# Optimization experiments

Hardware: AMD Instinct MI355X
Metric: run time of the kernel (lower is better)

The kernel has to match this reference:

```python
import jax, jax.numpy as jnp
import numpy as np

E = 304   # embedding size
H = 304   # hidden size
D = 61    # dict_size
B = 256   # batch
T = 512   # frame_num
P = 68    # max_phn_num


def _gru_cell(h, x, Wih, Whh, bih, bhh):
    # PyTorch GRU cell: gates ordered (r, z, n)
    gi = x @ Wih.T + bih            # [B, 3H]
    gh = h @ Whh.T + bhh            # [B, 3H]
    i_r, i_z, i_n = jnp.split(gi, 3, axis=-1)
    h_r, h_z, h_n = jnp.split(gh, 3, axis=-1)
    r = jax.nn.sigmoid(i_r + h_r)
    z = jax.nn.sigmoid(i_z + h_z)
    n = jnp.tanh(i_n + r * h_n)
    return (1.0 - z) * n + z * h


def _run_gru(xs, h0, Wih, Whh, bih, bhh):
    # xs: [B, L, E] -> outputs [B, L, H], final hidden [B, H]
    def step(h, x):
        h = _gru_cell(h, x, Wih, Whh, bih, bhh)
        return h, h
    h_last, outs = jax.lax.scan(step, h0, jnp.swapaxes(xs, 0, 1))
    return jnp.swapaxes(outs, 0, 1), h_last


def setup_inputs() -> dict:
    key = jax.random.key(0)
    ks = jax.random.split(key, 12)
    s = 1.0 / np.sqrt(H)
    u = lambda k, shp: jax.random.uniform(k, shp, jnp.float32, -s, s)
    return {
        'input': jax.random.normal(ks[0], (B, T, E), jnp.float32),
        'target': jax.random.randint(ks[1], (B, P, 1), 0, D),
        'teacher_forcing': 1,
        'enc_Wih': u(ks[2], (3 * H, E)),
        'enc_Whh': u(ks[3], (3 * H, H)),
        'enc_bih': u(ks[4], (3 * H,)),
        'enc_bhh': u(ks[5], (3 * H,)),
        'emb': jax.random.normal(ks[6], (D, E), jnp.float32),
        'dec_Wih': u(ks[7], (3 * H, E)),
        'dec_Whh': u(ks[8], (3 * H, H)),
        'dec_bih': u(ks[9], (3 * H,)),
        'dec_bhh': u(ks[10], (3 * H,)),
        'lin_W': u(ks[11], (D, H)),
        'lin_b': jnp.zeros((D,), jnp.float32),
    }


def reference(input, target, teacher_forcing, enc_Wih, enc_Whh, enc_bih, enc_bhh,
              emb, dec_Wih, dec_Whh, dec_bih, dec_bhh, lin_W, lin_b):
    batch = input.shape[0]
    h0 = jnp.zeros((batch, H), input.dtype)
    # Encoder: the python loop over frames is mathematically a full GRU scan
    enc_outs, enc_h = _run_gru(input, h0, enc_Wih, enc_Whh, enc_bih, enc_bhh)
    # Decoder (teacher_forcing == 1): input tokens are [0, target[:,1], ..., target[:,P-1]]
    toks = jnp.concatenate(
        [jnp.zeros((batch, 1), target.dtype), target[:, 1:, 0]], axis=1)  # [B, P]
    dec_x = emb[toks]                                                      # [B, P, E]
    dec_outs, _ = _run_gru(dec_x, enc_h, dec_Wih, dec_Whh, dec_bih, dec_bhh)
    logits = dec_outs @ lin_W.T + lin_b        # [B, P, D]
    softmaxs = jax.nn.softmax(logits, axis=-1)
    softmax_cal = softmaxs[:, :-1, :].reshape(-1, D)
    target_cal = target[:, 1:, :].reshape(-1)
    asr_outputs = jnp.argmax(softmaxs[:, :-1, :], axis=2)[:, :, None]
    return softmax_cal, target_cal, asr_outputs
```

## Files before the change

### kernel.cpp

```cpp
#include <hip/hip_runtime.h>
#include <math.h>

#define B_   256
#define E_   304
#define H_   304
#define T_   512
#define P_   68
#define PD   67
#define D_   61
#define NCB  16
#define NBG  16
#define RB   16
#define CBH  19
#define GC   57
#define NSTEP (T_ + PD)
#define HW   152
#define BLK_ULL (RB * HW)
#define LROW 328
#define LROWU 164
#define NKS  10
#define SC_LO 2048.0f
#define SC_INV 4.8828125e-4f

typedef unsigned long long ull;
typedef _Float16 half8 __attribute__((ext_vector_type(8)));
typedef _Float16 half2v __attribute__((ext_vector_type(2)));
typedef float f32x4 __attribute__((ext_vector_type(4)));

__global__ __launch_bounds__(256, 1) void gru_persist(
    const float* __restrict__ input,
    const int*   __restrict__ target,
    const float* __restrict__ emb,
    const float* __restrict__ eWih, const float* __restrict__ eWhh,
    const float* __restrict__ ebih, const float* __restrict__ ebhh,
    const float* __restrict__ dWih, const float* __restrict__ dWhh,
    const float* __restrict__ dbih, const float* __restrict__ dbhh,
    float* hbuf,
    float* __restrict__ dec_outs,
    int* ctr)
{
    __shared__ _Float16 opH[2][RB * LROW];
    __shared__ _Float16 opL[2][RB * LROW];
    __shared__ float red0[64 * 17], red1[64 * 17];
    __shared__ float bi_l[2][GC], bh_l[2][GC];

    const int tid  = threadIdx.x;
    const int L    = blockIdx.x;
    const int xcd  = L & 7;
    const int yy   = L >> 3;
    const int cb   = yy & 15;
    const int bg   = ((yy >> 4) << 3) | xcd;
    const int r0   = bg * RB;
    const int c0h  = cb * CBH;
    const int wv   = tid >> 6;
    const int lane = tid & 63;
    int* ctrp = ctr + bg * 32;

    half8 wih_h[NKS], wih_l[NKS], whh_h[NKS], whh_l[NKS];

    auto packw = [&](const float* W, half8* wh, half8* wl) {
        int c = wv * 16 + (lane & 15);
        bool valid = (c < GC);
        int g = valid ? c / CBH : 0, j19 = valid ? c - (c / CBH) * CBH : 0;
        const float* wp = W + (size_t)(g * H_ + c0h + j19) * 304;
        int grp = (lane >> 4) * 8;
        #pragma unroll
        for (int ks = 0; ks < NKS; ++ks) {
            half8 vh, vl;
            #pragma unroll
            for (int j = 0; j < 8; ++j) {
                int k = ks * 32 + grp + j;
                float v = (valid && k < 304) ? wp[k] : 0.f;
                _Float16 hi = (_Float16)v;
                float rres = v - (float)hi;
                vh[j] = hi;
                vl[j] = (_Float16)(rres * SC_LO);
            }
            wh[ks] = vh; wl[ks] = vl;
        }
    };

    auto gemm = [&](const _Float16* aH, const _Float16* aL,
                    const half8* wh, const half8* wl, float* red) {
        const int base = (lane & 15) * LROW + (lane >> 4) * 8;
        f32x4 a0 = {0.f, 0.f, 0.f, 0.f}, a1 = a0, a2 = a0;
        #pragma unroll
        for (int ks = 0; ks < NKS; ++ks) {
            half8 Ah = *(const half8*)&aH[base + ks * 32];
            half8 Al = *(const half8*)&aL[base + ks * 32];
            a0 = __builtin_amdgcn_mfma_f32_16x16x32_f16(Ah, wh[ks], a0, 0, 0, 0);
            a1 = __builtin_amdgcn_mfma_f32_16x16x32_f16(Ah, wl[ks], a1, 0, 0, 0);
            a2 = __builtin_amdgcn_mfma_f32_16x16x32_f16(Al, wh[ks], a2, 0, 0, 0);
        }
        f32x4 r = a0 + (a1 + a2) * SC_INV;
        int rb = (wv * 16 + (lane & 15)) * 17 + (lane >> 4) * 4;
        #pragma unroll
        for (int i = 0; i < 4; ++i) red[rb + i] = r[i];
    };

    auto cvtstore = [&](ull u, int plane, int idx) {
        float a0 = __uint_as_float((unsigned)u);
        float a1 = __uint_as_float((unsigned)(u >> 32));
        _Float16 h0 = (_Float16)a0, h1 = (_Float16)a1;
        float r0f = a0 - (float)h0, r1f = a1 - (float)h1;
        half2v vh; vh.x = h0; vh.y = h1;
        half2v vl; vl.x = (_Float16)(r0f * SC_LO); vl.y = (_Float16)(r1f * SC_LO);
        ((half2v*)&opH[plane][0])[idx] = vh;
        ((half2v*)&opL[plane][0])[idx] = vl;
    };

    packw(eWih, wih_h, wih_l);
    packw(eWhh, whh_h, whh_l);
    if (tid < GC) {
        int g = tid / CBH, j = tid - (tid / CBH) * CBH;
        bi_l[0][tid] = ebih[g * H_ + c0h + j];
        bh_l[0][tid] = ebhh[g * H_ + c0h + j];
        bi_l[1][tid] = dbih[g * H_ + c0h + j];
        bh_l[1][tid] = dbhh[g * H_ + c0h + j];
    }

    for (int f = tid; f < RB * LROW; f += 256) {
        ((unsigned*)opH)[f] = 0u;
        ((unsigned*)opL)[f] = 0u;
    }
    __syncthreads();
    {
        const ull* xin = (const ull*)input;
        #pragma unroll
        for (int i = 0; i < 10; ++i) {
            int f = tid + 256 * i;
            if (i < 9 || f < BLK_ULL) {
                int rr = f / HW, q = f - (f / HW) * HW;
                cvtstore(xin[(size_t)(r0 + rr) * T_ * HW + q], 0, rr * LROWU + q);
            }
        }
    }
    __syncthreads();
    gemm(opH[0], opL[0], wih_h, wih_l, red0);
    ull xr[10];
    {
        const ull* xin = (const ull*)input;
        #pragma unroll
        for (int i = 0; i < 10; ++i) {
            int f = tid + 256 * i;
            if (i < 9 || f < BLK_ULL) {
                int rr = f / HW, q = f - (f / HW) * HW;
                xr[i] = xin[((size_t)(r0 + rr) * T_ + 1) * HW + q];
            }
        }
    }

    for (int s = 0; s < NSTEP; ++s) {
        __syncthreads();
        const bool enc = (s < T_);
        if (s == T_) packw(dWhh, whh_h, whh_l);

        ull hreg[10];
        if (s > 0) {
            const ull* hsrc = (const ull*)(hbuf + (size_t)(s & 1) * (B_ * H_))
                              + (size_t)r0 * HW;
            #pragma unroll
            for (int i = 0; i < 10; ++i) {
                int f = tid + 256 * i;
                if (i < 9 || f < BLK_ULL)
                    hreg[i] = __hip_atomic_load(hsrc + f, __ATOMIC_RELAXED,
                                                __HIP_MEMORY_SCOPE_AGENT);
            }
        }
        if (s + 1 < NSTEP) {
            #pragma unroll
            for (int i = 0; i < 10; ++i) {
                int f = tid + 256 * i;
                if (i < 9 || f < BLK_ULL) {
                    int rr = f / HW, q = f - (f / HW) * HW;
                    cvtstore(xr[i], 0, rr * LROWU + q);
                }
            }
        }
        if (s > 0) {
            #pragma unroll
            for (int i = 0; i < 10; ++i) {
                int f = tid + 256 * i;
                if (i < 9 || f < BLK_ULL) {
                    int rr = f / HW, q = f - (f / HW) * HW;
                    cvtstore(hreg[i], 1, rr * LROWU + q);
                }
            }
        }
        if (s + 2 < NSTEP) {
            if (s + 2 < T_) {
                const ull* xin = (const ull*)input;
                #pragma unroll
                for (int i = 0; i < 10; ++i) {
                    int f = tid + 256 * i;
                    if (i < 9 || f < BLK_ULL) {
                        int rr = f / HW, q = f - (f / HW) * HW;
                        xr[i] = xin[((size_t)(r0 + rr) * T_ + (s + 2)) * HW + q];
                    }
                }
            } else {
                const ull* eb = (const ull*)emb;
                int p2 = s + 2 - T_;
                #pragma unroll
                for (int i = 0; i < 10; ++i) {
                    int f = tid + 256 * i;
                    if (i < 9 || f < BLK_ULL) {
                        int rr = f / HW, q = f - (f / HW) * HW;
                        int tok = (p2 == 0) ? 0 : target[(r0 + rr) * P_ + p2];
                        xr[i] = eb[(size_t)tok * HW + q];
                    }
                }
            }
        }
        __syncthreads();

        gemm(opH[1], opL[1], whh_h, whh_l, red1);
        __syncthreads();

        float* hdst = hbuf + (size_t)((s + 1) & 1) * (B_ * H_);
        for (int o = tid; o < RB * CBH; o += 256) {
            int rr = o / CBH, j = o - (o / CBH) * CBH;
            int col = c0h + j;
            int ph = enc ? 0 : 1;
            float Gi[3], Gh[3];
            #pragma unroll
            for (int g = 0; g < 3; ++g) {
                int c = g * CBH + j;
                Gi[g] = red0[c * 17 + rr] + bi_l[ph][c];
                Gh[g] = red1[c * 17 + rr] + bh_l[ph][c];
            }
            float rg = 1.f / (1.f + expf(-(Gi[0] + Gh[0])));
            float zg = 1.f / (1.f + expf(-(Gi[1] + Gh[1])));
            float ng = tanhf(Gi[2] + rg * Gh[2]);
            float hv = (float)opH[1][rr * LROW + col]
                     + (float)opL[1][rr * LROW + col] * SC_INV;
            float hnew = (1.f - zg) * ng + zg * hv;
            __hip_atomic_store(&hdst[(size_t)(r0 + rr) * H_ + col], hnew,
                               __ATOMIC_RELAXED, __HIP_MEMORY_SCOPE_AGENT);
            if (!enc)
                dec_outs[((size_t)(r0 + rr) * PD + (s - T_)) * H_ + col] = hnew;
        }
        __syncthreads();

        if (s + 1 < NSTEP) {
            if (tid == 0)
                __hip_atomic_fetch_add(ctrp, 1, __ATOMIC_RELAXED,
                                       __HIP_MEMORY_SCOPE_AGENT);
            if (s + 1 == T_) packw(dWih, wih_h, wih_l);
            gemm(opH[0], opL[0], wih_h, wih_l, red0);
            if (tid == 0) {
                int tgt = NCB * (s + 1);
                while (__hip_atomic_load(ctrp, __ATOMIC_RELAXED,
                                         __HIP_MEMORY_SCOPE_AGENT) < tgt)
                    __builtin_amdgcn_s_sleep(1);
            }
        }
    }
}

__global__ __launch_bounds__(256) void logits_softmax(
    const float* __restrict__ dec_outs,
    const float* __restrict__ linW,
    const float* __restrict__ linb,
    const int* __restrict__ target,
    float* __restrict__ out)
{
    __shared__ float wsm[H_][64];
    __shared__ float rs[4][H_];
    const int tid = threadIdx.x;
    const int wv = tid >> 6, l = tid & 63;

    for (int f = tid; f < H_ * 64; f += 256) {
        int k = f >> 6, ll = f & 63;
        wsm[k][ll] = (ll < D_) ? linW[(size_t)ll * H_ + k] : 0.f;
    }
    const int r = blockIdx.x * 4 + wv;
    const float* rowp = dec_outs + (size_t)r * H_;
    for (int k = l; k < H_; k += 64) rs[wv][k] = rowp[k];
    __syncthreads();

    float acc = -1e30f;
    if (l < D_) {
        acc = linb[l];
        #pragma unroll 4
        for (int k = 0; k < H_; ++k) acc += rs[wv][k] * wsm[k][l];
    }
    float m = acc;
    for (int off = 32; off; off >>= 1) m = fmaxf(m, __shfl_xor(m, off));
    float e = (l < D_) ? expf(acc - m) : 0.f;
    float s = e;
    for (int off = 32; off; off >>= 1) s += __shfl_xor(s, off);
    float av = acc; int ai = l;
    for (int off = 32; off; off >>= 1) {
        float ov = __shfl_xor(av, off);
        int oi = __shfl_xor(ai, off);
        if (ov > av || (ov == av && oi < ai)) { av = ov; ai = oi; }
    }
    const int b = r / PD, p = r - (r / PD) * PD;
    const size_t OFF1 = (size_t)B_ * PD * D_;
    const size_t OFF2 = OFF1 + (size_t)B_ * PD;
    if (l < D_)        out[(size_t)r * D_ + l] = e / s;
    else if (l == D_)  out[OFF1 + r] = (float)target[b * P_ + p + 1];
    else if (l == D_ + 1) out[OFF2 + r] = (float)ai;
}

extern "C" void kernel_launch(void* const* d_in, const int* in_sizes, int n_in,
                              void* d_out, int out_size, void* d_ws, size_t ws_size,
                              hipStream_t stream)
{
    const float* input  = (const float*)d_in[0];
    const int*   target = (const int*)d_in[1];
    const float* eWih = (const float*)d_in[3];
    const float* eWhh = (const float*)d_in[4];
    const float* ebih = (const float*)d_in[5];
    const float* ebhh = (const float*)d_in[6];
    const float* emb  = (const float*)d_in[7];
    const float* dWih = (const float*)d_in[8];
    const float* dWhh = (const float*)d_in[9];
    const float* dbih = (const float*)d_in[10];
    const float* dbhh = (const float*)d_in[11];
    const float* linW = (const float*)d_in[12];
    const float* linb = (const float*)d_in[13];
    float* out = (float*)d_out;

    int*   ctr      = (int*)d_ws;
    float* hbuf     = (float*)d_ws + 1024;
    float* dec_outs = hbuf + 2 * (size_t)B_ * H_;

    (void)hipMemsetAsync(ctr, 0, 1024 * sizeof(int), stream);

    gru_persist<<<dim3(256), 256, 0, stream>>>(
        input, target, emb,
        eWih, eWhh, ebih, ebhh,
        dWih, dWhh, dbih, dbhh,
        hbuf, dec_outs, ctr);

    logits_softmax<<<dim3(B_ * PD / 4), 256, 0, stream>>>(
        dec_outs, linW, linb, target, out);
}
```

Measured before the change: 2.390 ms.

## Replace group counter barrier with per-slice flags and pre-split fp16 hidden exchange

Each producer block now writes its hidden-state slice already split into fp16 hi/lo halves packed in one 32-bit word, and raises its own per-slice flag. It no longer increments a shared counter that a single thread spins on. Consumer wavefronts each poll the flags of the slices they need and copy them straight into LDS, so the global barrier wait overlaps with gathering data and the per-element fp32-to-fp16 split moves to the producer. The reduction buffer stride also changes so the GEMM results can be written with one vector store. The relaxed atomics still carry no acquire/release fences, so memory ordering rests on the same assumptions as before.

```diff
diff --git a/kernel.cpp b/kernel.cpp
--- a/kernel.cpp
+++ b/kernel.cpp
@@ -19,6 +19,9 @@
 #define LROW 328
 #define LROWU 164
 #define NKS  10
+#define SLICE 304
+#define SLICEP 320
+#define RSTR 20
 #define SC_LO 2048.0f
 #define SC_INV 4.8828125e-4f
 
@@ -35,13 +38,13 @@
     const float* __restrict__ ebih, const float* __restrict__ ebhh,
     const float* __restrict__ dWih, const float* __restrict__ dWhh,
     const float* __restrict__ dbih, const float* __restrict__ dbhh,
-    float* hbuf,
-    float* __restrict__ dec_outs,
-    int* ctr)
+    unsigned* xbuf,
+    int* flg,
+    float* __restrict__ dec_outs)
 {
     __shared__ _Float16 opH[2][RB * LROW];
     __shared__ _Float16 opL[2][RB * LROW];
-    __shared__ float red0[64 * 17], red1[64 * 17];
+    __shared__ float red0[64 * RSTR], red1[64 * RSTR];
     __shared__ float bi_l[2][GC], bh_l[2][GC];
 
     const int tid  = threadIdx.x;
@@ -54,7 +57,6 @@
     const int c0h  = cb * CBH;
     const int wv   = tid >> 6;
     const int lane = tid & 63;
-    int* ctrp = ctr + bg * 32;
 
     half8 wih_h[NKS], wih_l[NKS], whh_h[NKS], whh_l[NKS];
 
@@ -93,9 +95,8 @@
             a2 = __builtin_amdgcn_mfma_f32_16x16x32_f16(Al, wh[ks], a2, 0, 0, 0);
         }
         f32x4 r = a0 + (a1 + a2) * SC_INV;
-        int rb = (wv * 16 + (lane & 15)) * 17 + (lane >> 4) * 4;
-        #pragma unroll
-        for (int i = 0; i < 4; ++i) red[rb + i] = r[i];
+        int rb = (wv * 16 + (lane & 15)) * RSTR + (lane >> 4) * 4;
+        *(f32x4*)&red[rb] = r;
     };
 
     auto cvtstore = [&](ull u, int plane, int idx) {
@@ -155,18 +156,6 @@
         const bool enc = (s < T_);
         if (s == T_) packw(dWhh, whh_h, whh_l);
 
-        ull hreg[10];
-        if (s > 0) {
-            const ull* hsrc = (const ull*)(hbuf + (size_t)(s & 1) * (B_ * H_))
-                              + (size_t)r0 * HW;
-            #pragma unroll
-            for (int i = 0; i < 10; ++i) {
-                int f = tid + 256 * i;
-                if (i < 9 || f < BLK_ULL)
-                    hreg[i] = __hip_atomic_load(hsrc + f, __ATOMIC_RELAXED,
-                                                __HIP_MEMORY_SCOPE_AGENT);
-            }
-        }
         if (s + 1 < NSTEP) {
             #pragma unroll
             for (int i = 0; i < 10; ++i) {
@@ -174,16 +163,6 @@
                 if (i < 9 || f < BLK_ULL) {
                     int rr = f / HW, q = f - (f / HW) * HW;
                     cvtstore(xr[i], 0, rr * LROWU + q);
-                }
-            }
-        }
-        if (s > 0) {
-            #pragma unroll
-            for (int i = 0; i < 10; ++i) {
-                int f = tid + 256 * i;
-                if (i < 9 || f < BLK_ULL) {
-                    int rr = f / HW, q = f - (f / HW) * HW;
-                    cvtstore(hreg[i], 1, rr * LROWU + q);
                 }
             }
         }
@@ -212,12 +191,40 @@
                 }
             }
         }
+        if (s > 0) {
+            const unsigned* xb = xbuf
+                + ((size_t)(s & 1) * NBG * NCB + (size_t)bg * NCB) * SLICEP;
+            for (int k = 0; k < 4; ++k) {
+                const int sl = wv + 4 * k;
+                const int* fp = flg + (bg * NCB + sl) * 16;
+                while (__hip_atomic_load(fp, __ATOMIC_RELAXED,
+                                         __HIP_MEMORY_SCOPE_AGENT) < s)
+                    __builtin_amdgcn_s_sleep(1);
+                __builtin_amdgcn_sched_barrier(0);
+                const unsigned* sp = xb + (size_t)sl * SLICEP;
+                #pragma unroll
+                for (int p = 0; p < 5; ++p) {
+                    int e = lane + 64 * p;
+                    if (e < SLICE) {
+                        unsigned u = __hip_atomic_load(sp + e, __ATOMIC_RELAXED,
+                                                       __HIP_MEMORY_SCOPE_AGENT);
+                        int rr = e / CBH, j = e - (e / CBH) * CBH;
+                        int idx = rr * LROW + sl * CBH + j;
+                        opH[1][idx] = __builtin_bit_cast(_Float16,
+                                          (unsigned short)(u & 0xffffu));
+                        opL[1][idx] = __builtin_bit_cast(_Float16,
+                                          (unsigned short)(u >> 16));
+                    }
+                }
+            }
+        }
         __syncthreads();
 
         gemm(opH[1], opL[1], whh_h, whh_l, red1);
         __syncthreads();
 
-        float* hdst = hbuf + (size_t)((s + 1) & 1) * (B_ * H_);
+        unsigned* xdst = xbuf
+            + ((size_t)((s + 1) & 1) * NBG * NCB + (size_t)bg * NCB + cb) * SLICEP;
         for (int o = tid; o < RB * CBH; o += 256) {
             int rr = o / CBH, j = o - (o / CBH) * CBH;
             int col = c0h + j;
@@ -226,8 +233,8 @@
             #pragma unroll
             for (int g = 0; g < 3; ++g) {
                 int c = g * CBH + j;
-                Gi[g] = red0[c * 17 + rr] + bi_l[ph][c];
-                Gh[g] = red1[c * 17 + rr] + bh_l[ph][c];
+                Gi[g] = red0[c * RSTR + rr] + bi_l[ph][c];
+                Gh[g] = red1[c * RSTR + rr] + bh_l[ph][c];
             }
             float rg = 1.f / (1.f + expf(-(Gi[0] + Gh[0])));
             float zg = 1.f / (1.f + expf(-(Gi[1] + Gh[1])));
@@ -235,8 +242,14 @@
             float hv = (float)opH[1][rr * LROW + col]
                      + (float)opL[1][rr * LROW + col] * SC_INV;
             float hnew = (1.f - zg) * ng + zg * hv;
-            __hip_atomic_store(&hdst[(size_t)(r0 + rr) * H_ + col], hnew,
-                               __ATOMIC_RELAXED, __HIP_MEMORY_SCOPE_AGENT);
+            _Float16 hh = (_Float16)hnew;
+            float res = hnew - (float)hh;
+            unsigned short hb = __builtin_bit_cast(unsigned short, hh);
+            unsigned short lb = __builtin_bit_cast(unsigned short,
+                                    (_Float16)(res * SC_LO));
+            unsigned pk = ((unsigned)lb << 16) | hb;
+            __hip_atomic_store(xdst + o, pk, __ATOMIC_RELAXED,
+                               __HIP_MEMORY_SCOPE_AGENT);
             if (!enc)
                 dec_outs[((size_t)(r0 + rr) * PD + (s - T_)) * H_ + col] = hnew;
         }
@@ -244,16 +257,10 @@
 
         if (s + 1 < NSTEP) {
             if (tid == 0)
-                __hip_atomic_fetch_add(ctrp, 1, __ATOMIC_RELAXED,
-                                       __HIP_MEMORY_SCOPE_AGENT);
+                __hip_atomic_store(flg + (bg * NCB + cb) * 16, s + 1,
+                                   __ATOMIC_RELAXED, __HIP_MEMORY_SCOPE_AGENT);
             if (s + 1 == T_) packw(dWih, wih_h, wih_l);
             gemm(opH[0], opL[0], wih_h, wih_l, red0);
-            if (tid == 0) {
-                int tgt = NCB * (s + 1);
-                while (__hip_atomic_load(ctrp, __ATOMIC_RELAXED,
-                                         __HIP_MEMORY_SCOPE_AGENT) < tgt)
-                    __builtin_amdgcn_s_sleep(1);
-            }
         }
     }
 }
@@ -323,17 +330,17 @@
     const float* linb = (const float*)d_in[13];
     float* out = (float*)d_out;
 
-    int*   ctr      = (int*)d_ws;
-    float* hbuf     = (float*)d_ws + 1024;
-    float* dec_outs = hbuf + 2 * (size_t)B_ * H_;
-
-    (void)hipMemsetAsync(ctr, 0, 1024 * sizeof(int), stream);
+    int*      flg      = (int*)d_ws;
+    unsigned* xbuf     = (unsigned*)d_ws + NBG * NCB * 16;
+    float*    dec_outs = (float*)((unsigned*)xbuf + 2 * NBG * NCB * SLICEP);
+
+    (void)hipMemsetAsync(flg, 0, NBG * NCB * 16 * sizeof(int), stream);
 
     gru_persist<<<dim3(256), 256, 0, stream>>>(
         input, target, emb,
         eWih, eWhh, ebih, ebhh,
         dWih, dWhh, dbih, dbhh,
-        hbuf, dec_outs, ctr);
+        xbuf, flg, dec_outs);
 
     logits_softmax<<<dim3(B_ * PD / 4), 256, 0, stream>>>(
         dec_outs, linW, linb, target, out);
```

Measured after the change: 5.571 ms. +133.1%, slower.

## Replace shared atomic counter barrier with per-block flags polled by a wavefront

Applied to the files above, without the earlier changes.

Swaps the per-batch-group atomic fetch_add counter for one flag per block, each on its own 64-byte slot. Each block stores its step number, and one wavefront polls all 16 peer flags in parallel, using __all to decide when to proceed. This removes serialized atomic RMW contention on a single counter line in the per-step inter-block barrier of the persistent GRU loop. It also pads the reduction buffer stride to 20 so the four accumulator values go out as one vector store instead of four scalar stores.

```diff
diff --git a/kernel.cpp b/kernel.cpp
--- a/kernel.cpp
+++ b/kernel.cpp
@@ -19,6 +19,7 @@
 #define LROW 328
 #define LROWU 164
 #define NKS  10
+#define RSTR 20
 #define SC_LO 2048.0f
 #define SC_INV 4.8828125e-4f
 
@@ -37,11 +38,11 @@
     const float* __restrict__ dbih, const float* __restrict__ dbhh,
     float* hbuf,
     float* __restrict__ dec_outs,
-    int* ctr)
+    int* flg)
 {
     __shared__ _Float16 opH[2][RB * LROW];
     __shared__ _Float16 opL[2][RB * LROW];
-    __shared__ float red0[64 * 17], red1[64 * 17];
+    __shared__ float red0[64 * RSTR], red1[64 * RSTR];
     __shared__ float bi_l[2][GC], bh_l[2][GC];
 
     const int tid  = threadIdx.x;
@@ -54,7 +55,6 @@
     const int c0h  = cb * CBH;
     const int wv   = tid >> 6;
     const int lane = tid & 63;
-    int* ctrp = ctr + bg * 32;
 
     half8 wih_h[NKS], wih_l[NKS], whh_h[NKS], whh_l[NKS];
 
@@ -93,9 +93,8 @@
             a2 = __builtin_amdgcn_mfma_f32_16x16x32_f16(Al, wh[ks], a2, 0, 0, 0);
         }
         f32x4 r = a0 + (a1 + a2) * SC_INV;
-        int rb = (wv * 16 + (lane & 15)) * 17 + (lane >> 4) * 4;
-        #pragma unroll
-        for (int i = 0; i < 4; ++i) red[rb + i] = r[i];
+        int rb = (wv * 16 + (lane & 15)) * RSTR + (lane >> 4) * 4;
+        *(f32x4*)&red[rb] = r;
     };
 
     auto cvtstore = [&](ull u, int plane, int idx) {
@@ -226,8 +225,8 @@
             #pragma unroll
             for (int g = 0; g < 3; ++g) {
                 int c = g * CBH + j;
-                Gi[g] = red0[c * 17 + rr] + bi_l[ph][c];
-                Gh[g] = red1[c * 17 + rr] + bh_l[ph][c];
+                Gi[g] = red0[c * RSTR + rr] + bi_l[ph][c];
+                Gh[g] = red1[c * RSTR + rr] + bh_l[ph][c];
             }
             float rg = 1.f / (1.f + expf(-(Gi[0] + Gh[0])));
             float zg = 1.f / (1.f + expf(-(Gi[1] + Gh[1])));
@@ -244,15 +243,21 @@
 
         if (s + 1 < NSTEP) {
             if (tid == 0)
-                __hip_atomic_fetch_add(ctrp, 1, __ATOMIC_RELAXED,
-                                       __HIP_MEMORY_SCOPE_AGENT);
+                __hip_atomic_store(flg + (bg * NCB + cb) * 16, s + 1,
+                                   __ATOMIC_RELAXED, __HIP_MEMORY_SCOPE_AGENT);
             if (s + 1 == T_) packw(dWih, wih_h, wih_l);
             gemm(opH[0], opL[0], wih_h, wih_l, red0);
-            if (tid == 0) {
-                int tgt = NCB * (s + 1);
-                while (__hip_atomic_load(ctrp, __ATOMIC_RELAXED,
-                                         __HIP_MEMORY_SCOPE_AGENT) < tgt)
+            if (wv == 0) {
+                const int tgt = s + 1;
+                const int* fp = flg + (bg * NCB + (lane & 15)) * 16;
+                for (;;) {
+                    int f = (lane < NCB)
+                        ? __hip_atomic_load(fp, __ATOMIC_RELAXED,
+                                            __HIP_MEMORY_SCOPE_AGENT)
+                        : tgt;
+                    if (__all(f >= tgt)) break;
                     __builtin_amdgcn_s_sleep(1);
+                }
             }
         }
     }
@@ -323,17 +328,17 @@
     const float* linb = (const float*)d_in[13];
     float* out = (float*)d_out;
 
-    int*   ctr      = (int*)d_ws;
-    float* hbuf     = (float*)d_ws + 1024;
+    int*   flg      = (int*)d_ws;
+    float* hbuf     = (float*)d_ws + NBG * NCB * 16;
     float* dec_outs = hbuf + 2 * (size_t)B_ * H_;
 
-    (void)hipMemsetAsync(ctr, 0, 1024 * sizeof(int), stream);
+    (void)hipMemsetAsync(flg, 0, NBG * NCB * 16 * sizeof(int), stream);
 
     gru_persist<<<dim3(256), 256, 0, stream>>>(
         input, target, emb,
         eWih, eWhh, ebih, ebhh,
         dWih, dWhh, dbih, dbhh,
-        hbuf, dec_outs, ctr);
+        hbuf, dec_outs, flg);
 
     logits_softmax<<<dim3(B_ * PD / 4), 256, 0, stream>>>(
         dec_outs, linW, linb, target, out);
```

Result: no change. 2.390 ms, median of 2 (+0.0%).
